# Kernel optimization log

Measured on AMD Instinct MI355X. Metric: run time of the kernel, lower is better.

Reference implementation:

```python
import jax, jax.numpy as jnp
import numpy as np

# Model config (matches init_kwargs)
D_MODEL = 1536
NUM_HEADS = 16
QUERY_GROUPS = 4
HEAD_DIM = D_MODEL // NUM_HEADS  # 96
HEADS_PER_GROUP = NUM_HEADS // QUERY_GROUPS
ROPE_THETA = 10000.0
B, T, GH, GW = 2, 16, 16, 16
S = GH * GW  # spatial patches per frame
QKV_OUT = NUM_HEADS * HEAD_DIM + 2 * QUERY_GROUPS * HEAD_DIM  # 2304


def setup_inputs() -> dict:
    key = jax.random.key(0)
    k1, k2, k3 = jax.random.split(key, 3)
    x = jax.random.normal(k1, (B, T, S, D_MODEL), dtype=jnp.float32)
    padding_mask = jnp.ones((B * T, S), dtype=jnp.int32)
    # nn.Linear weights stored as [out, in]; y = x @ W.T
    w_qkv = jax.random.normal(k2, (QKV_OUT, D_MODEL), dtype=jnp.float32) * (1.0 / np.sqrt(D_MODEL))
    w_o = jax.random.normal(k3, (D_MODEL, D_MODEL), dtype=jnp.float32) * (1.0 / np.sqrt(D_MODEL))
    return {"x": x, "padding_mask": padding_mask, "w_qkv": w_qkv, "w_o": w_o}


def _rot_half(seg, cos, sin):
    # seg: [..., d]; half-split rotary rotation
    d = seg.shape[-1] // 2
    x1, x2 = seg[..., :d], seg[..., d:]
    return jnp.concatenate([x1 * cos - x2 * sin, x1 * sin + x2 * cos], axis=-1)


def _cos_sin(pos, seg_dim):
    # pos: [L] -> cos/sin [L, seg_dim//2]
    inv_freq = 1.0 / (ROPE_THETA ** (jnp.arange(seg_dim // 2, dtype=jnp.float32) * 2.0 / seg_dim))
    ang = pos.astype(jnp.float32)[:, None] * inv_freq[None, :]
    return jnp.cos(ang), jnp.sin(ang)


def _apply_rope3d(x):
    # x: [B*T, S, heads, HEAD_DIM]; head_dim split equally over (t, h, w) axes
    seg = HEAD_DIM // 3  # 32
    t_pos = jnp.tile(jnp.arange(T), B)            # [B*T] temporal index per attention-batch row
    h_pos = jnp.repeat(jnp.arange(GH), GW)        # [S]
    w_pos = jnp.tile(jnp.arange(GW), GH)          # [S]
    ct, st = _cos_sin(t_pos, seg)  # [B*T, seg/2]
    ch, sh = _cos_sin(h_pos, seg)  # [S, seg/2]
    cw, sw = _cos_sin(w_pos, seg)
    xt = _rot_half(x[..., :seg], ct[:, None, None, :], st[:, None, None, :])
    xh = _rot_half(x[..., seg:2 * seg], ch[None, :, None, :], sh[None, :, None, :])
    xw = _rot_half(x[..., 2 * seg:], cw[None, :, None, :], sw[None, :, None, :])
    return jnp.concatenate([xt, xh, xw], axis=-1)


def reference(x, padding_mask, w_qkv, w_o):
    # Spatial attention mode: [B, T, S, D] -> [B*T, S, D]
    xs = x.reshape(B * T, S, D_MODEL)
    qkv = jnp.einsum('bsd,od->bso', xs, w_qkv)  # [B*T, S, QKV_OUT]
    q_end = NUM_HEADS * HEAD_DIM
    k_end = q_end + QUERY_GROUPS * HEAD_DIM
    q = qkv[..., :q_end].reshape(B * T, S, NUM_HEADS, HEAD_DIM)
    k = qkv[..., q_end:k_end].reshape(B * T, S, QUERY_GROUPS, HEAD_DIM)
    v = qkv[..., k_end:].reshape(B * T, S, QUERY_GROUPS, HEAD_DIM)
    # RoPE3D on q and k
    q = _apply_rope3d(q)
    k = _apply_rope3d(k)
    # GQA: extend kv heads to num_heads (repeat_interleave)
    k = jnp.repeat(k, HEADS_PER_GROUP, axis=2)  # [B*T, S, NUM_HEADS, HEAD_DIM]
    v = jnp.repeat(v, HEADS_PER_GROUP, axis=2)
    scale = 1.0 / np.sqrt(HEAD_DIM)
    scores = jnp.einsum('bqhd,bkhd->bhqk', q, k) * scale  # [B*T, H, S, S]
    mask = (padding_mask != 0)[:, None, None, :]  # [B*T, 1, 1, S], True = attend
    scores = jnp.where(mask, scores, jnp.float32(-1e9))
    probs = jax.nn.softmax(scores, axis=-1)
    attn = jnp.einsum('bhqk,bkhd->bqhd', probs, v).reshape(B * T, S, D_MODEL)
    out = jnp.einsum('bsd,od->bso', attn, w_o)
    return out.reshape(B, T, S, D_MODEL)
```

## Files before the change

### kernel.cpp

```cpp
#include <hip/hip_runtime.h>
#include <hip/hip_bf16.h>
#include <stdint.h>

typedef __attribute__((ext_vector_type(8))) short short8;
typedef __attribute__((ext_vector_type(4))) float f32x4;
typedef __attribute__((ext_vector_type(4))) float f4;
typedef __attribute__((ext_vector_type(4))) short s4;
typedef __attribute__((ext_vector_type(4))) uint u4;

typedef __attribute__((address_space(1))) const void gvoid_t;
typedef __attribute__((address_space(3))) void lvoid_t;

__device__ __forceinline__ void gload_lds16(const void* g, void* l) {
  __builtin_amdgcn_global_load_lds((gvoid_t*)g, (lvoid_t*)l, 16, 0, 0);
}

__device__ __forceinline__ ushort f2b(float f) {
  union { float f; uint32_t u; } v; v.f = f;
  return (ushort)((v.u + 0x7fffu + ((v.u >> 16) & 1u)) >> 16);
}
__device__ __forceinline__ float b2f(ushort b) {
  union { uint32_t u; float f; } v; v.u = ((uint32_t)b) << 16;
  return v.f;
}
__device__ __forceinline__ uint cvtpk(float lo, float hi) {
  uint r;
  asm volatile("v_cvt_pk_bf16_f32 %0, %1, %2" : "=v"(r) : "v"(lo), "v"(hi));
  return r;
}

template <int N> __device__ __forceinline__ void wait_vmcnt();
template <> __device__ __forceinline__ void wait_vmcnt<0>() { asm volatile("s_waitcnt vmcnt(0)" ::: "memory"); }

__device__ __forceinline__ void wait_lgkm0() {
  asm volatile("s_waitcnt lgkmcnt(0)" ::: "memory");
  __builtin_amdgcn_sched_barrier(0);
}
__device__ __forceinline__ void barrier_fence() {
  asm volatile("s_barrier" ::: "memory");
}

__global__ void prep2_kernel(const float* __restrict__ wq, const float* __restrict__ wo,
                             ushort* __restrict__ Wq, ushort* __restrict__ Wo,
                             float2* __restrict__ tab) {
  int b = blockIdx.x, tid = threadIdx.x;
  const float* in; ushort* out; int i;
  if (b < 3456)      { in = wq; out = Wq; i = b * 256 + tid; }
  else if (b < 5760) { in = wo; out = Wo; i = (b - 3456) * 256 + tid; }
  else {
    int pos = tid >> 4, fi = tid & 15;
    float inv_freq = __expf(-(float)fi * 0.5756462732485115f);
    float ang = (float)pos * inv_freq;
    float sn, c;
    __sincosf(ang, &sn, &c);
    tab[tid] = make_float2(c, sn);
    return;
  }
  f4 v = ((const f4*)in)[i];
  s4 o;
  o.x = (short)f2b(v.x); o.y = (short)f2b(v.y);
  o.z = (short)f2b(v.z); o.w = (short)f2b(v.w);
  ((s4*)out)[i] = o;
}

__global__ __launch_bounds__(512, 2) void gemm6x(const float* __restrict__ Af,
                                                 const ushort* __restrict__ B,
                                                 ushort* __restrict__ C) {
  constexpr int BN = 288, NF = 9, RB = 144;
  constexpr int K = 1536, NT = 24;
  constexpr int ABUF = 256 * 64;
  constexpr int BBUF = BN * 64;
  constexpr uint ABYTE = ABUF * 2;
  constexpr uint BBYTE = BBUF * 2;
  constexpr int BRND = 4, BTW = 4;

  __shared__ ushort As[2 * ABUF];
  __shared__ ushort Bs[2 * BBUF];

  const int tid = threadIdx.x;
  const int l = tid & 63, w = tid >> 6;
  const int wr = w >> 1, wc = w & 1;
  const int r16 = l & 15, kh = l >> 4;
  const int sc = (l & 7) ^ (l >> 3);
  const int srow = w * 8 + (l >> 3);

  const int xcd = blockIdx.x & 7;
  const int ii = blockIdx.x >> 3;
  const int bm = xcd * 4 + (ii & 3);
  const int bn = ii >> 2;
  const float* Ag = Af + (size_t)bm * 256 * K;
  const ushort* Bg = B + (size_t)bn * BN * K;

  const char* AsR = (const char*)As;
  const char* BsR = (const char*)Bs;
  const uint khsw = ((uint)kh * 16) ^ ((uint)(r16 & 7) * 16);
  const uint PA = (uint)(wr * 64 + r16) * 128 + khsw;
  const uint PB = (uint)(wc * RB + r16) * 128 + khsw;

  const float* gaf[4];
  const ushort* gb[BRND];
  const ushort* gbt;
#pragma unroll
  for (int i = 0; i < 4; ++i) gaf[i] = Ag + (size_t)(i * 64 + srow) * K + sc * 8;
#pragma unroll
  for (int i = 0; i < BRND; ++i) gb[i] = Bg + (size_t)(i * 64 + srow) * K + sc * 8;
  gbt = Bg + (size_t)(BRND * 64 + srow) * K + sc * 8;

  const uint adst = (uint)w * 512 + (uint)l * 8;

  {
    f4 p0[4], p1[4];
#pragma unroll
    for (int i = 0; i < 4; ++i) {
      p0[i] = *((const f4*)gaf[i]);
      p1[i] = *((const f4*)gaf[i] + 1);
    }
#pragma unroll
    for (int i = 0; i < 4; ++i) {
      u4 pk;
      pk.x = cvtpk(p0[i].x, p0[i].y);
      pk.y = cvtpk(p0[i].z, p0[i].w);
      pk.z = cvtpk(p1[i].x, p1[i].y);
      pk.w = cvtpk(p1[i].z, p1[i].w);
      *(u4*)(&As[i * 4096 + adst]) = pk;
    }
  }
#pragma unroll
  for (int i = 0; i < BRND; ++i) gload_lds16(gb[i], Bs + i * 4096 + w * 512);
  if (w < BTW) gload_lds16(gbt, Bs + BRND * 4096 + w * 512);
#pragma unroll
  for (int i = 0; i < BRND; ++i) gb[i] += 64;
  gbt += 64;
  wait_vmcnt<0>();
  wait_lgkm0();
  barrier_fence();

  f32x4 acc[4][NF] = {};
  short8 afr[4], bfr[NF];
  f4 a0[4], a1[4];

  for (int u = 0; u < NT; ++u) {
    const int cur = u & 1;
    const uint aoff = cur ? ABYTE : 0u;
    const uint boff = cur ? BBYTE : 0u;
    ushort* An = As + (cur ^ 1) * ABUF;
    ushort* Bn = Bs + (cur ^ 1) * BBUF;
    const bool st = (u + 1 < NT);
    const int kt1 = (u + 1) * 64;

    {
      const uint pa = PA + aoff, pb = PB + boff;
#pragma unroll
      for (int m = 0; m < 4; ++m) afr[m] = *(const short8*)(AsR + pa + m * 2048);
#pragma unroll
      for (int n = 0; n < NF; ++n) bfr[n] = *(const short8*)(BsR + pb + n * 2048);
    }
    if (st) {
#pragma unroll
      for (int i = 0; i < 4; ++i) {
        a0[i] = *((const f4*)(gaf[i] + kt1));
        a1[i] = *((const f4*)(gaf[i] + kt1) + 1);
      }
    }
    wait_lgkm0();
    __builtin_amdgcn_s_setprio(1);
#pragma unroll
    for (int m = 0; m < 4; ++m)
#pragma unroll
      for (int n = 0; n < NF; ++n)
        acc[m][n] = __builtin_amdgcn_mfma_f32_16x16x32_bf16(afr[m], bfr[n], acc[m][n], 0, 0, 0);
    __builtin_amdgcn_s_setprio(0);

    {
      const uint pa = (PA ^ 64u) + aoff, pb = (PB ^ 64u) + boff;
#pragma unroll
      for (int m = 0; m < 4; ++m) afr[m] = *(const short8*)(AsR + pa + m * 2048);
#pragma unroll
      for (int n = 0; n < NF; ++n) bfr[n] = *(const short8*)(BsR + pb + n * 2048);
    }
    if (st) {
#pragma unroll
      for (int i = 0; i < 4; ++i) {
        u4 pk;
        pk.x = cvtpk(a0[i].x, a0[i].y);
        pk.y = cvtpk(a0[i].z, a0[i].w);
        pk.z = cvtpk(a1[i].x, a1[i].y);
        pk.w = cvtpk(a1[i].z, a1[i].w);
        *(u4*)(&An[i * 4096 + adst]) = pk;
      }
#pragma unroll
      for (int i = 0; i < BRND; ++i) gload_lds16(gb[i], Bn + i * 4096 + w * 512);
      if (w < BTW) gload_lds16(gbt, Bn + BRND * 4096 + w * 512);
#pragma unroll
      for (int i = 0; i < BRND; ++i) gb[i] += 64;
      gbt += 64;
    }
    wait_lgkm0();
    __builtin_amdgcn_s_setprio(1);
#pragma unroll
    for (int m = 0; m < 4; ++m)
#pragma unroll
      for (int n = 0; n < NF; ++n)
        acc[m][n] = __builtin_amdgcn_mfma_f32_16x16x32_bf16(afr[m], bfr[n], acc[m][n], 0, 0, 0);
    __builtin_amdgcn_s_setprio(0);

    wait_vmcnt<0>();
    barrier_fence();
  }

  const int rowb = bm * 256 + wr * 64;
  const int colb = bn * BN + wc * RB;
#pragma unroll
  for (int m = 0; m < 4; ++m)
#pragma unroll
    for (int n = 0; n < NF; ++n)
#pragma unroll
      for (int r = 0; r < 4; ++r) {
        int row = rowb + m * 16 + kh * 4 + r;
        int col = colb + n * 16 + r16;
        C[(size_t)row * 2304 + col] = f2b(acc[m][n][r]);
      }
}

template <int BN, typename OutT>
__global__ __launch_bounds__(512, 2) void gemm6(const ushort* __restrict__ A,
                                                const ushort* __restrict__ B,
                                                OutT* __restrict__ C,
                                                int N, int K) {
  constexpr int NF = BN / 32;
  constexpr int RB = BN / 2;
  constexpr int ABUF = 256 * 64;
  constexpr int BBUF = BN * 64;
  constexpr uint ABYTE = ABUF * 2;
  constexpr uint BBYTE = BBUF * 2;
  constexpr int BRND = BN / 64;
  constexpr int BTW = (BN % 64) / 8;

  __shared__ ushort As[2 * ABUF];
  __shared__ ushort Bs[2 * BBUF];

  const int tid = threadIdx.x;
  const int l = tid & 63, w = tid >> 6;
  const int wr = w >> 1, wc = w & 1;
  const int r16 = l & 15, kh = l >> 4;
  const int sc = (l & 7) ^ (l >> 3);
  const int srow = w * 8 + (l >> 3);

  const int xcd = blockIdx.x & 7;
  const int ii = blockIdx.x >> 3;
  const int bm = xcd * 4 + (ii & 3);
  const int bn = ii >> 2;
  const ushort* Ag = A + (size_t)bm * 256 * K;
  const ushort* Bg = B + (size_t)bn * BN * K;
  const int NT = K >> 6;

  const char* AsR = (const char*)As;
  const char* BsR = (const char*)Bs;
  const uint khsw = ((uint)kh * 16) ^ ((uint)(r16 & 7) * 16);
  const uint PA = (uint)(wr * 64 + r16) * 128 + khsw;
  const uint PB = (uint)(wc * RB + r16) * 128 + khsw;

  const ushort* ga[4];
  const ushort* gb[BRND];
  const ushort* gbt = nullptr;
#pragma unroll
  for (int i = 0; i < 4; ++i) ga[i] = Ag + (size_t)(i * 64 + srow) * K + sc * 8;
#pragma unroll
  for (int i = 0; i < BRND; ++i) gb[i] = Bg + (size_t)(i * 64 + srow) * K + sc * 8;
  if constexpr (BTW > 0) gbt = Bg + (size_t)(BRND * 64 + srow) * K + sc * 8;

#pragma unroll
  for (int i = 0; i < 4; ++i) gload_lds16(ga[i], As + i * 4096 + w * 512);
#pragma unroll
  for (int i = 0; i < BRND; ++i) gload_lds16(gb[i], Bs + i * 4096 + w * 512);
  if constexpr (BTW > 0) { if (w < BTW) gload_lds16(gbt, Bs + BRND * 4096 + w * 512); }
#pragma unroll
  for (int i = 0; i < 4; ++i) ga[i] += 64;
#pragma unroll
  for (int i = 0; i < BRND; ++i) gb[i] += 64;
  if constexpr (BTW > 0) gbt += 64;
  wait_vmcnt<0>();
  barrier_fence();

  f32x4 acc[4][NF] = {};
  short8 afr[4], bfr[NF];

  for (int u = 0; u < NT; ++u) {
    const int cur = u & 1;
    const uint aoff = cur ? ABYTE : 0u;
    const uint boff = cur ? BBYTE : 0u;
    ushort* An = As + (cur ^ 1) * ABUF;
    ushort* Bn = Bs + (cur ^ 1) * BBUF;
    const bool st = (u + 1 < NT);

    {
      const uint pa = PA + aoff, pb = PB + boff;
#pragma unroll
      for (int m = 0; m < 4; ++m) afr[m] = *(const short8*)(AsR + pa + m * 2048);
#pragma unroll
      for (int n = 0; n < NF; ++n) bfr[n] = *(const short8*)(BsR + pb + n * 2048);
    }
    if (st) {
#pragma unroll
      for (int i = 0; i < 4; ++i) gload_lds16(ga[i], An + i * 4096 + w * 512);
    }
    wait_lgkm0();
    __builtin_amdgcn_s_setprio(1);
#pragma unroll
    for (int m = 0; m < 4; ++m)
#pragma unroll
      for (int n = 0; n < NF; ++n)
        acc[m][n] = __builtin_amdgcn_mfma_f32_16x16x32_bf16(afr[m], bfr[n], acc[m][n], 0, 0, 0);
    __builtin_amdgcn_s_setprio(0);

    {
      const uint pa = (PA ^ 64u) + aoff, pb = (PB ^ 64u) + boff;
#pragma unroll
      for (int m = 0; m < 4; ++m) afr[m] = *(const short8*)(AsR + pa + m * 2048);
#pragma unroll
      for (int n = 0; n < NF; ++n) bfr[n] = *(const short8*)(BsR + pb + n * 2048);
    }
    if (st) {
#pragma unroll
      for (int i = 0; i < BRND; ++i) gload_lds16(gb[i], Bn + i * 4096 + w * 512);
      if constexpr (BTW > 0) { if (w < BTW) gload_lds16(gbt, Bn + BRND * 4096 + w * 512); }
    }
    wait_lgkm0();
    __builtin_amdgcn_s_setprio(1);
#pragma unroll
    for (int m = 0; m < 4; ++m)
#pragma unroll
      for (int n = 0; n < NF; ++n)
        acc[m][n] = __builtin_amdgcn_mfma_f32_16x16x32_bf16(afr[m], bfr[n], acc[m][n], 0, 0, 0);
    __builtin_amdgcn_s_setprio(0);

#pragma unroll
    for (int i = 0; i < 4; ++i) ga[i] += 64;
#pragma unroll
    for (int i = 0; i < BRND; ++i) gb[i] += 64;
    if constexpr (BTW > 0) gbt += 64;
    wait_vmcnt<0>();
    barrier_fence();
  }

  const int rowb = bm * 256 + wr * 64;
  const int colb = bn * BN + wc * RB;
#pragma unroll
  for (int m = 0; m < 4; ++m)
#pragma unroll
    for (int n = 0; n < NF; ++n)
#pragma unroll
      for (int r = 0; r < 4; ++r) {
        int row = rowb + m * 16 + kh * 4 + r;
        int col = colb + n * 16 + r16;
        float val = acc[m][n][r];
        if constexpr (sizeof(OutT) == 2) C[(size_t)row * N + col] = f2b(val);
        else                             C[(size_t)row * N + col] = val;
      }
}

__device__ __forceinline__ short8 shfl_xor32(short8 v) {
  union { short8 s; int i[4]; } a, b;
  a.s = v;
#pragma unroll
  for (int q = 0; q < 4; ++q) b.i[q] = __shfl_xor(a.i[q], 32, 64);
  return b.s;
}
__device__ __forceinline__ short8 rope_frag(short8 v, int pos, int kh, const float2* Tb) {
  short8 p = shfl_xor32(v);
  const float sgn = (kh < 2) ? -1.0f : 1.0f;
  const int ib = pos * 16 + (kh & 1) * 8;
  short8 o;
#pragma unroll
  for (int j = 0; j < 8; ++j) {
    float2 cs = Tb[ib + j];
    o[j] = (short)f2b(b2f((ushort)v[j]) * cs.x + sgn * b2f((ushort)p[j]) * cs.y);
  }
  return o;
}

__global__ __launch_bounds__(512, 1) void attn3_kernel(
    const ushort* __restrict__ QKV,
    const int* __restrict__ mask,
    const float2* __restrict__ Tab,
    ushort* __restrict__ Out) {
  __shared__ ushort Ks[256 * 104];
  __shared__ ushort Vs[96 * 264];
  __shared__ ushort Ps[8][16 * 136];
  __shared__ float Mb[256];
  __shared__ float2 Tb[256];

  const int b = blockIdx.x;
  const int qt = b & 1;
  const int g = (b >> 1) & 3;
  const int bt = b >> 3;
  const int t = threadIdx.x;
  const int l = t & 63, w = t >> 6;
  const int r16 = l & 15, kh = l >> 4;
  const int h = g * 4 + (w >> 1);
  const int qc = w & 1;
  const int t0 = bt & 15;

  if (t < 256) { Tb[t] = Tab[t]; Mb[t] = mask[bt * 256 + t] ? 0.0f : -1.0e9f; }
  __syncthreads();

  {
    const int r = t >> 1, ch = t & 1;
    const ushort* src = QKV + (size_t)(bt * 256 + r) * 2304 + 1536 + g * 96;
    const int p1 = r >> 4, p2 = r & 15;
    if (ch == 0) {
      short8 v0 = *(const short8*)(src + 0);
      short8 v1 = *(const short8*)(src + 8);
      short8 v2 = *(const short8*)(src + 16);
      short8 v3 = *(const short8*)(src + 24);
      short8 o0, o1, o2, o3;
#pragma unroll
      for (int j = 0; j < 8; ++j) {
        float2 ca = Tb[t0 * 16 + j], cb = Tb[t0 * 16 + 8 + j];
        float x1a = b2f((ushort)v0[j]), x2a = b2f((ushort)v2[j]);
        float x1b = b2f((ushort)v1[j]), x2b = b2f((ushort)v3[j]);
        o0[j] = (short)f2b(x1a * ca.x - x2a * ca.y);
        o1[j] = (short)f2b(x1b * cb.x - x2b * cb.y);
        o2[j] = (short)f2b(x1a * ca.y + x2a * ca.x);
        o3[j] = (short)f2b(x1b * cb.y + x2b * cb.x);
      }
      *(short8*)(&Ks[r * 104 + 0])  = o0;
      *(short8*)(&Ks[r * 104 + 8])  = o1;
      *(short8*)(&Ks[r * 104 + 16]) = o2;
      *(short8*)(&Ks[r * 104 + 24]) = o3;
      v0 = *(const short8*)(src + 32);
      v1 = *(const short8*)(src + 40);
      v2 = *(const short8*)(src + 48);
      v3 = *(const short8*)(src + 56);
#pragma unroll
      for (int j = 0; j < 8; ++j) {
        float2 ca = Tb[p1 * 16 + j], cb = Tb[p1 * 16 + 8 + j];
        float x1a = b2f((ushort)v0[j]), x2a = b2f((ushort)v2[j]);
        float x1b = b2f((ushort)v1[j]), x2b = b2f((ushort)v3[j]);
        o0[j] = (short)f2b(x1a * ca.x - x2a * ca.y);
        o1[j] = (short)f2b(x1b * cb.x - x2b * cb.y);
        o2[j] = (short)f2b(x1a * ca.y + x2a * ca.x);
        o3[j] = (short)f2b(x1b * cb.y + x2b * cb.x);
      }
      *(short8*)(&Ks[r * 104 + 32]) = o0;
      *(short8*)(&Ks[r * 104 + 40]) = o1;
      *(short8*)(&Ks[r * 104 + 48]) = o2;
      *(short8*)(&Ks[r * 104 + 56]) = o3;
    } else {
      short8 v0 = *(const short8*)(src + 64);
      short8 v1 = *(const short8*)(src + 72);
      short8 v2 = *(const short8*)(src + 80);
      short8 v3 = *(const short8*)(src + 88);
      short8 o0, o1, o2, o3;
#pragma unroll
      for (int j = 0; j < 8; ++j) {
        float2 ca = Tb[p2 * 16 + j], cb = Tb[p2 * 16 + 8 + j];
        float x1a = b2f((ushort)v0[j]), x2a = b2f((ushort)v2[j]);
        float x1b = b2f((ushort)v1[j]), x2b = b2f((ushort)v3[j]);
        o0[j] = (short)f2b(x1a * ca.x - x2a * ca.y);
        o1[j] = (short)f2b(x1b * cb.x - x2b * cb.y);
        o2[j] = (short)f2b(x1a * ca.y + x2a * ca.x);
        o3[j] = (short)f2b(x1b * cb.y + x2b * cb.x);
      }
      *(short8*)(&Ks[r * 104 + 64]) = o0;
      *(short8*)(&Ks[r * 104 + 72]) = o1;
      *(short8*)(&Ks[r * 104 + 80]) = o2;
      *(short8*)(&Ks[r * 104 + 88]) = o3;
    }
  }

#pragma unroll
  for (int i = 0; i < 6; ++i) {
    int c = t + i * 512;
    int s = c / 12, dq = c - s * 12;
    short8 vv = *(const short8*)(QKV + (size_t)(bt * 256 + s) * 2304 + 1920 + g * 96 + dq * 8);
#pragma unroll
    for (int j = 0; j < 8; ++j)
      Vs[(dq * 8 + j) * 264 + s] = (ushort)vv[j];
  }
  __syncthreads();

  const ushort* Qp = QKV + (size_t)(bt * 256 + qt * 128 + qc * 64) * 2304 + h * 96;
  ushort* Pw = &Ps[w][0];
  const float scale = 0.10206207261596575f;

#pragma unroll
  for (int mp = 0; mp < 2; ++mp) {
    const int qb = mp * 32;
    const int p1A = qt * 8 + qc * 4 + mp * 2;
    const int p1B = p1A + 1;

    short8 qfA[3], qfB[3];
    {
      short8 rA0 = *(const short8*)(Qp + (size_t)(qb + r16) * 2304 + 0 + kh * 8);
      short8 rA1 = *(const short8*)(Qp + (size_t)(qb + r16) * 2304 + 32 + kh * 8);
      short8 rA2 = *(const short8*)(Qp + (size_t)(qb + r16) * 2304 + 64 + kh * 8);
      short8 rB0 = *(const short8*)(Qp + (size_t)(qb + 16 + r16) * 2304 + 0 + kh * 8);
      short8 rB1 = *(const short8*)(Qp + (size_t)(qb + 16 + r16) * 2304 + 32 + kh * 8);
      short8 rB2 = *(const short8*)(Qp + (size_t)(qb + 16 + r16) * 2304 + 64 + kh * 8);
      qfA[0] = rope_frag(rA0, t0, kh, Tb);
      qfA[1] = rope_frag(rA1, p1A, kh, Tb);
      qfA[2] = rope_frag(rA2, r16, kh, Tb);
      qfB[0] = rope_frag(rB0, t0, kh, Tb);
      qfB[1] = rope_frag(rB1, p1B, kh, Tb);
      qfB[2] = rope_frag(rB2, r16, kh, Tb);
    }

    f32x4 scA[16] = {}, scB[16] = {};
#pragma unroll
    for (int f = 0; f < 16; ++f) {
#pragma unroll
      for (int kc = 0; kc < 3; ++kc) {
        short8 kf = *(const short8*)(&Ks[(f * 16 + r16) * 104 + kc * 32 + kh * 8]);
        scA[f] = __builtin_amdgcn_mfma_f32_16x16x32_bf16(qfA[kc], kf, scA[f], 0, 0, 0);
        scB[f] = __builtin_amdgcn_mfma_f32_16x16x32_bf16(qfB[kc], kf, scB[f], 0, 0, 0);
      }
    }

#pragma unroll
    for (int f = 0; f < 16; ++f) {
      float mb = Mb[f * 16 + r16];
#pragma unroll
      for (int r = 0; r < 4; ++r) {
        scA[f][r] = scA[f][r] * scale + mb;
        scB[f][r] = scB[f][r] * scale + mb;
      }
    }

    float invA[4], invB[4];
#pragma unroll
    for (int reg = 0; reg < 4; ++reg) {
      float mxA = -3.0e38f, mxB = -3.0e38f;
#pragma unroll
      for (int f = 0; f < 16; ++f) { mxA = fmaxf(mxA, scA[f][reg]); mxB = fmaxf(mxB, scB[f][reg]); }
      for (int o = 8; o >= 1; o >>= 1) { mxA = fmaxf(mxA, __shfl_xor(mxA, o, 64)); mxB = fmaxf(mxB, __shfl_xor(mxB, o, 64)); }
      float smA = 0.f, smB = 0.f;
#pragma unroll
      for (int f = 0; f < 16; ++f) {
        float pA = __expf(scA[f][reg] - mxA);
        float pB = __expf(scB[f][reg] - mxB);
        scA[f][reg] = pA; scB[f][reg] = pB;
        smA += pA; smB += pB;
      }
      for (int o = 8; o >= 1; o >>= 1) { smA += __shfl_xor(smA, o, 64); smB += __shfl_xor(smB, o, 64); }
      invA[reg] = 1.0f / smA;
      invB[reg] = 1.0f / smB;
    }

    short8 pfA[8], pfB[8];
#pragma unroll
    for (int ck = 0; ck < 2; ++ck) {
#pragma unroll
      for (int f = 0; f < 8; ++f)
#pragma unroll
        for (int reg = 0; reg < 4; ++reg)
          Pw[(kh * 4 + reg) * 136 + f * 16 + r16] = f2b(scA[ck * 8 + f][reg]);
#pragma unroll
      for (int kc = 0; kc < 4; ++kc)
        pfA[ck * 4 + kc] = *(const short8*)(&Pw[r16 * 136 + kc * 32 + kh * 8]);
    }
#pragma unroll
    for (int ck = 0; ck < 2; ++ck) {
#pragma unroll
      for (int f = 0; f < 8; ++f)
#pragma unroll
        for (int reg = 0; reg < 4; ++reg)
          Pw[(kh * 4 + reg) * 136 + f * 16 + r16] = f2b(scB[ck * 8 + f][reg]);
#pragma unroll
      for (int kc = 0; kc < 4; ++kc)
        pfB[ck * 4 + kc] = *(const short8*)(&Pw[r16 * 136 + kc * 32 + kh * 8]);
    }

    f32x4 oA[6] = {}, oB[6] = {};
#pragma unroll
    for (int dt = 0; dt < 6; ++dt) {
#pragma unroll
      for (int kc = 0; kc < 8; ++kc) {
        short8 vf = *(const short8*)(&Vs[(dt * 16 + r16) * 264 + kc * 32 + kh * 8]);
        oA[dt] = __builtin_amdgcn_mfma_f32_16x16x32_bf16(pfA[kc], vf, oA[dt], 0, 0, 0);
        oB[dt] = __builtin_amdgcn_mfma_f32_16x16x32_bf16(pfB[kc], vf, oB[dt], 0, 0, 0);
      }
    }

    const int rbase = bt * 256 + qt * 128 + qc * 64 + qb;
#pragma unroll
    for (int dt = 0; dt < 6; ++dt)
#pragma unroll
      for (int reg = 0; reg < 4; ++reg) {
        int col = h * 96 + dt * 16 + r16;
        Out[(size_t)(rbase + kh * 4 + reg) * 1536 + col]      = f2b(oA[dt][reg] * invA[reg]);
        Out[(size_t)(rbase + 16 + kh * 4 + reg) * 1536 + col] = f2b(oB[dt][reg] * invB[reg]);
      }
  }
}

extern "C" void kernel_launch(void* const* d_in, const int* in_sizes, int n_in,
                              void* d_out, int out_size, void* d_ws, size_t ws_size,
                              hipStream_t stream) {
  const float* x     = (const float*)d_in[0];
  const int* pmask   = (const int*)d_in[1];
  const float* w_qkv = (const float*)d_in[2];
  const float* w_o   = (const float*)d_in[3];
  float* out = (float*)d_out;

  char* ws = (char*)d_ws;
  ushort* Wq   = (ushort*)(ws + 0);
  ushort* Wo   = (ushort*)(ws + 7077888);
  ushort* QKV  = (ushort*)(ws + 11796480);
  float2* Tab  = (float2*)(ws + 49545216);
  ushort* Attn = (ushort*)(ws + 49547264);

  prep2_kernel<<<5761, 256, 0, stream>>>(w_qkv, w_o, Wq, Wo, Tab);

  gemm6x<<<256, 512, 0, stream>>>(x, Wq, QKV);

  attn3_kernel<<<256, 512, 0, stream>>>(QKV, pmask, Tab, Attn);

  gemm6<192, float><<<256, 512, 0, stream>>>(Attn, Wo, out, 1536, 1536);
}
```

Before: 144.4 us.

## Prefetch fp32 A tiles two stages ahead in QKV GEMM pipeline

Restructures the QKV GEMM main loop so the fp32 activation loads for tile u+2 are issued during iteration u and kept in registers, while tile u+1 is converted to bf16 and written to LDS at the start of the iteration. Partial vmcnt waits let B-tile LDS loads finish while A prefetches stay in flight. The aim is to hide global load latency of the fp32 A operand behind MFMA work, at the cost of longer register live ranges and reliance on the exact count of outstanding loads for the vmcnt(8) wait.

After: 141.8 us (median of 2 runs). Within noise of the previous version (-1.8%).

```diff
diff --git a/kernel.cpp b/kernel.cpp
--- a/kernel.cpp
+++ b/kernel.cpp
@@ -31,6 +31,7 @@
 
 template <int N> __device__ __forceinline__ void wait_vmcnt();
 template <> __device__ __forceinline__ void wait_vmcnt<0>() { asm volatile("s_waitcnt vmcnt(0)" ::: "memory"); }
+template <> __device__ __forceinline__ void wait_vmcnt<8>() { asm volatile("s_waitcnt vmcnt(8)" ::: "memory"); }
 
 __device__ __forceinline__ void wait_lgkm0() {
   asm volatile("s_waitcnt lgkmcnt(0)" ::: "memory");
@@ -108,22 +109,22 @@
 
   const uint adst = (uint)w * 512 + (uint)l * 8;
 
-  {
-    f4 p0[4], p1[4];
-#pragma unroll
-    for (int i = 0; i < 4; ++i) {
-      p0[i] = *((const f4*)gaf[i]);
-      p1[i] = *((const f4*)gaf[i] + 1);
-    }
-#pragma unroll
-    for (int i = 0; i < 4; ++i) {
-      u4 pk;
-      pk.x = cvtpk(p0[i].x, p0[i].y);
-      pk.y = cvtpk(p0[i].z, p0[i].w);
-      pk.z = cvtpk(p1[i].x, p1[i].y);
-      pk.w = cvtpk(p1[i].z, p1[i].w);
-      *(u4*)(&As[i * 4096 + adst]) = pk;
-    }
+  f4 a0[4], a1[4];
+
+#pragma unroll
+  for (int i = 0; i < 4; ++i) {
+    a0[i] = *((const f4*)gaf[i]);
+    a1[i] = *((const f4*)gaf[i] + 1);
+  }
+  wait_vmcnt<0>();
+#pragma unroll
+  for (int i = 0; i < 4; ++i) {
+    u4 pk;
+    pk.x = cvtpk(a0[i].x, a0[i].y);
+    pk.y = cvtpk(a0[i].z, a0[i].w);
+    pk.z = cvtpk(a1[i].x, a1[i].y);
+    pk.w = cvtpk(a1[i].z, a1[i].w);
+    *(u4*)(&As[i * 4096 + adst]) = pk;
   }
 #pragma unroll
   for (int i = 0; i < BRND; ++i) gload_lds16(gb[i], Bs + i * 4096 + w * 512);
@@ -131,13 +132,17 @@
 #pragma unroll
   for (int i = 0; i < BRND; ++i) gb[i] += 64;
   gbt += 64;
-  wait_vmcnt<0>();
+#pragma unroll
+  for (int i = 0; i < 4; ++i) {
+    a0[i] = *((const f4*)(gaf[i] + 64));
+    a1[i] = *((const f4*)(gaf[i] + 64) + 1);
+  }
+  wait_vmcnt<8>();
   wait_lgkm0();
   barrier_fence();
 
   f32x4 acc[4][NF] = {};
   short8 afr[4], bfr[NF];
-  f4 a0[4], a1[4];
 
   for (int u = 0; u < NT; ++u) {
     const int cur = u & 1;
@@ -145,8 +150,9 @@
     const uint boff = cur ? BBYTE : 0u;
     ushort* An = As + (cur ^ 1) * ABUF;
     ushort* Bn = Bs + (cur ^ 1) * BBUF;
-    const bool st = (u + 1 < NT);
-    const int kt1 = (u + 1) * 64;
+    const bool st1 = (u + 1 < NT);
+    const bool st2 = (u + 2 < NT);
+    const int kt2 = (u + 2) * 64;
 
     {
       const uint pa = PA + aoff, pb = PB + boff;
@@ -155,30 +161,9 @@
 #pragma unroll
       for (int n = 0; n < NF; ++n) bfr[n] = *(const short8*)(BsR + pb + n * 2048);
     }
-    if (st) {
-#pragma unroll
-      for (int i = 0; i < 4; ++i) {
-        a0[i] = *((const f4*)(gaf[i] + kt1));
-        a1[i] = *((const f4*)(gaf[i] + kt1) + 1);
-      }
-    }
-    wait_lgkm0();
-    __builtin_amdgcn_s_setprio(1);
-#pragma unroll
-    for (int m = 0; m < 4; ++m)
-#pragma unroll
-      for (int n = 0; n < NF; ++n)
-        acc[m][n] = __builtin_amdgcn_mfma_f32_16x16x32_bf16(afr[m], bfr[n], acc[m][n], 0, 0, 0);
-    __builtin_amdgcn_s_setprio(0);
-
-    {
-      const uint pa = (PA ^ 64u) + aoff, pb = (PB ^ 64u) + boff;
-#pragma unroll
-      for (int m = 0; m < 4; ++m) afr[m] = *(const short8*)(AsR + pa + m * 2048);
-#pragma unroll
-      for (int n = 0; n < NF; ++n) bfr[n] = *(const short8*)(BsR + pb + n * 2048);
-    }
-    if (st) {
+    if (st1) {
+      wait_vmcnt<0>();
+      __builtin_amdgcn_sched_barrier(0);
 #pragma unroll
       for (int i = 0; i < 4; ++i) {
         u4 pk;
@@ -188,12 +173,6 @@
         pk.w = cvtpk(a1[i].z, a1[i].w);
         *(u4*)(&An[i * 4096 + adst]) = pk;
       }
-#pragma unroll
-      for (int i = 0; i < BRND; ++i) gload_lds16(gb[i], Bn + i * 4096 + w * 512);
-      if (w < BTW) gload_lds16(gbt, Bn + BRND * 4096 + w * 512);
-#pragma unroll
-      for (int i = 0; i < BRND; ++i) gb[i] += 64;
-      gbt += 64;
     }
     wait_lgkm0();
     __builtin_amdgcn_s_setprio(1);
@@ -204,7 +183,38 @@
         acc[m][n] = __builtin_amdgcn_mfma_f32_16x16x32_bf16(afr[m], bfr[n], acc[m][n], 0, 0, 0);
     __builtin_amdgcn_s_setprio(0);
 
-    wait_vmcnt<0>();
+    {
+      const uint pa = (PA ^ 64u) + aoff, pb = (PB ^ 64u) + boff;
+#pragma unroll
+      for (int m = 0; m < 4; ++m) afr[m] = *(const short8*)(AsR + pa + m * 2048);
+#pragma unroll
+      for (int n = 0; n < NF; ++n) bfr[n] = *(const short8*)(BsR + pb + n * 2048);
+    }
+    if (st1) {
+#pragma unroll
+      for (int i = 0; i < BRND; ++i) gload_lds16(gb[i], Bn + i * 4096 + w * 512);
+      if (w < BTW) gload_lds16(gbt, Bn + BRND * 4096 + w * 512);
+#pragma unroll
+      for (int i = 0; i < BRND; ++i) gb[i] += 64;
+      gbt += 64;
+    }
+    if (st2) {
+#pragma unroll
+      for (int i = 0; i < 4; ++i) {
+        a0[i] = *((const f4*)(gaf[i] + kt2));
+        a1[i] = *((const f4*)(gaf[i] + kt2) + 1);
+      }
+    }
+    wait_lgkm0();
+    __builtin_amdgcn_s_setprio(1);
+#pragma unroll
+    for (int m = 0; m < 4; ++m)
+#pragma unroll
+      for (int n = 0; n < NF; ++n)
+        acc[m][n] = __builtin_amdgcn_mfma_f32_16x16x32_bf16(afr[m], bfr[n], acc[m][n], 0, 0, 0);
+    __builtin_amdgcn_s_setprio(0);
+
+    if (st2) wait_vmcnt<8>(); else wait_vmcnt<0>();
     barrier_fence();
   }
 
```
